# Optimization experiments

Hardware: AMD Instinct MI355X
Metric: run time of the kernel (lower is better)

Reference implementation:

```python
import jax, jax.numpy as jnp
import numpy as np

EPS = 1.0  # args.eps
N, D, H = 2097152, 2, 4

_PARAM_SPECS = [
    ("w_xin", (H, D)), ("b_xin", (H,)),
    ("w_xp1", (H, H)), ("b_xp1", (H,)),
    ("w_xp2", (H, H)), ("b_xp2", (H,)),
    ("w_xl1", (H, D)), ("b_xl1", (H,)),
    ("w_xl2", (H, H)), ("b_xl2", (H,)),
    ("w_xl3", (H, H)), ("b_xl3", (H,)),
    ("w_xlo", (1, H)), ("b_xlo", (1,)),
    ("w_cp1", (H, H)),  # PositiveLinear, no bias
    ("w_cp2", (H, H)),
    ("w_cpo", (1, H)),
    ("w_cp1m", (H, H)), ("b_cp1m", (H,)),
    ("w_cp2m", (H, H)), ("b_cp2m", (H,)),
    ("w_cpom", (H, H)), ("b_cpom", (H,)),
    ("w_clin", (H, D)),  # no bias
    ("w_cl1", (H, D)),
    ("w_cl2", (H, D)),
    ("w_clo", (1, D)),
    ("w_clinm", (D, D)), ("b_clinm", (D,)),
    ("w_cl1m", (D, H)), ("b_cl1m", (D,)),
    ("w_cl2m", (D, H)), ("b_cl2m", (D,)),
    ("w_clom", (D, H)), ("b_clom", (D,)),
]

def setup_inputs() -> dict:
    key = jax.random.key(0)
    k_x, k_xs, k_p = jax.random.split(key, 3)
    inp = {
        "x": jax.random.normal(k_x, (N, D), dtype=jnp.float32),
        "x_star": jax.random.normal(k_xs, (N, D), dtype=jnp.float32),
    }
    pkeys = jax.random.split(k_p, len(_PARAM_SPECS))
    for (name, shape), k in zip(_PARAM_SPECS, pkeys):
        if name.startswith("b_"):
            inp[name] = jnp.zeros(shape, dtype=jnp.float32)  # zeros bias init
        else:
            fan_in = shape[1]
            std = np.sqrt(2.0 / fan_in).astype(np.float32)  # kaiming normal
            inp[name] = jax.random.normal(k, shape, dtype=jnp.float32) * std
    return inp

def _lin(x, W, b=None):
    y = x @ W.T
    return y + b if b is not None else y

def _plin(x, W):
    # PositiveLinear reparam: W>=0 -> W + exp(-eps); W<0 -> exp(W - eps)
    Wr = jnp.where(W >= 0, W + jnp.exp(jnp.float32(-EPS)), jnp.exp(W - EPS))
    return x @ Wr.T

def reference(x, x_star,
              w_xin, b_xin, w_xp1, b_xp1, w_xp2, b_xp2,
              w_xl1, b_xl1, w_xl2, b_xl2, w_xl3, b_xl3, w_xlo, b_xlo,
              w_cp1, w_cp2, w_cpo,
              w_cp1m, b_cp1m, w_cp2m, b_cp2m, w_cpom, b_cpom,
              w_clin, w_cl1, w_cl2, w_clo,
              w_clinm, b_clinm, w_cl1m, b_cl1m, w_cl2m, b_cl2m, w_clom, b_clom):
    sp = jax.nn.softplus
    x0, x0s = x, x_star
    xs = sp(_lin(x0, w_xl1, b_xl1) + _lin(x0s * _lin(x0, w_clinm, b_clinm), w_clin))
    xh = sp(_lin(x0, w_xin, b_xin))
    xs = sp(_lin(xh, w_xl2, b_xl2)
            + _plin(xs * sp(_lin(xh, w_cp1m, b_cp1m)), w_cp1)
            + _lin(x0s * _lin(xh, w_cl1m, b_cl1m), w_cl1))
    xh = sp(_lin(xh, w_xp1, b_xp1))
    xs = sp(_lin(xh, w_xl3, b_xl3)
            + _plin(xs * sp(_lin(xh, w_cp2m, b_cp2m)), w_cp2)
            + _lin(x0s * _lin(xh, w_cl2m, b_cl2m), w_cl2))
    xh = sp(_lin(xh, w_xp2, b_xp2))
    out = sp(_lin(xh, w_xlo, b_xlo)
             + _plin(xs * sp(_lin(xh, w_cpom, b_cpom)), w_cpo)
             + _lin(x0s * _lin(xh, w_clom, b_clom), w_clo))
    return out  # [N, 1]
```

## Files before the change

kernel.cpp:

```cpp
#include <hip/hip_runtime.h>
#include <hip/hip_bf16.h>


#define NROWS_PER_THREAD 4

__device__ __forceinline__ float sp(float v) {
    float e = __expf(-fabsf(v));
    return fmaxf(v, 0.0f) + __logf(1.0f + e);
}

__device__ __forceinline__ float posw(float w) {
    const float EXP_NEG1 = 0.36787944117144233f;
    return (w >= 0.0f) ? (w + EXP_NEG1) : __expf(w - 1.0f);
}

__device__ __forceinline__ void mid_stage(
    float xs[NROWS_PER_THREAD][4], float xh[NROWS_PER_THREAD][4],
    const float XS0[NROWS_PER_THREAD][2],
    const float* __restrict__ w_xl,  const float* __restrict__ b_xl,
    const float* __restrict__ w_cpm, const float* __restrict__ b_cpm,
    const float* __restrict__ w_cp,
    const float* __restrict__ w_clm, const float* __restrict__ b_clm,
    const float* __restrict__ w_cl,
    const float* __restrict__ w_xp,  const float* __restrict__ b_xp)
{
    float v[NROWS_PER_THREAD][4];
    #pragma unroll
    for (int h = 0; h < 4; ++h) {
        float w0 = w_cpm[h*4+0], w1 = w_cpm[h*4+1], w2 = w_cpm[h*4+2], w3 = w_cpm[h*4+3];
        float b  = b_cpm[h];
        #pragma unroll
        for (int r = 0; r < NROWS_PER_THREAD; ++r) {
            float m = sp(fmaf(w0, xh[r][0], fmaf(w1, xh[r][1], fmaf(w2, xh[r][2], fmaf(w3, xh[r][3], b)))));
            v[r][h] = xs[r][h] * m;
        }
    }
    float u[NROWS_PER_THREAD][2];
    #pragma unroll
    for (int d = 0; d < 2; ++d) {
        float w0 = w_clm[d*4+0], w1 = w_clm[d*4+1], w2 = w_clm[d*4+2], w3 = w_clm[d*4+3];
        float b  = b_clm[d];
        #pragma unroll
        for (int r = 0; r < NROWS_PER_THREAD; ++r) {
            float t = fmaf(w0, xh[r][0], fmaf(w1, xh[r][1], fmaf(w2, xh[r][2], fmaf(w3, xh[r][3], b))));
            u[r][d] = XS0[r][d] * t;
        }
    }
    float ns[NROWS_PER_THREAD][4];
    #pragma unroll
    for (int h = 0; h < 4; ++h) {
        float a0 = w_xl[h*4+0], a1 = w_xl[h*4+1], a2 = w_xl[h*4+2], a3 = w_xl[h*4+3];
        float ab = b_xl[h];
        float p0 = posw(w_cp[h*4+0]), p1 = posw(w_cp[h*4+1]);
        float p2 = posw(w_cp[h*4+2]), p3 = posw(w_cp[h*4+3]);
        float c0 = w_cl[h*2+0], c1 = w_cl[h*2+1];
        #pragma unroll
        for (int r = 0; r < NROWS_PER_THREAD; ++r) {
            float t = fmaf(a0, xh[r][0], fmaf(a1, xh[r][1], fmaf(a2, xh[r][2], fmaf(a3, xh[r][3], ab))));
            t = fmaf(p0, v[r][0], fmaf(p1, v[r][1], fmaf(p2, v[r][2], fmaf(p3, v[r][3], t))));
            t = fmaf(c0, u[r][0], fmaf(c1, u[r][1], t));
            ns[r][h] = sp(t);
        }
    }
    float nh[NROWS_PER_THREAD][4];
    #pragma unroll
    for (int h = 0; h < 4; ++h) {
        float w0 = w_xp[h*4+0], w1 = w_xp[h*4+1], w2 = w_xp[h*4+2], w3 = w_xp[h*4+3];
        float b  = b_xp[h];
        #pragma unroll
        for (int r = 0; r < NROWS_PER_THREAD; ++r)
            nh[r][h] = sp(fmaf(w0, xh[r][0], fmaf(w1, xh[r][1], fmaf(w2, xh[r][2], fmaf(w3, xh[r][3], b)))));
    }
    #pragma unroll
    for (int r = 0; r < NROWS_PER_THREAD; ++r)
        #pragma unroll
        for (int h = 0; h < 4; ++h) { xs[r][h] = ns[r][h]; xh[r][h] = nh[r][h]; }
}

__global__ __launch_bounds__(256)
void dissip_kernel(
    const float* __restrict__ x,      const float* __restrict__ xst,
    const float* __restrict__ w_xin,  const float* __restrict__ b_xin,
    const float* __restrict__ w_xp1,  const float* __restrict__ b_xp1,
    const float* __restrict__ w_xp2,  const float* __restrict__ b_xp2,
    const float* __restrict__ w_xl1,  const float* __restrict__ b_xl1,
    const float* __restrict__ w_xl2,  const float* __restrict__ b_xl2,
    const float* __restrict__ w_xl3,  const float* __restrict__ b_xl3,
    const float* __restrict__ w_xlo,  const float* __restrict__ b_xlo,
    const float* __restrict__ w_cp1,  const float* __restrict__ w_cp2,
    const float* __restrict__ w_cpo,
    const float* __restrict__ w_cp1m, const float* __restrict__ b_cp1m,
    const float* __restrict__ w_cp2m, const float* __restrict__ b_cp2m,
    const float* __restrict__ w_cpom, const float* __restrict__ b_cpom,
    const float* __restrict__ w_clin, const float* __restrict__ w_cl1,
    const float* __restrict__ w_cl2,  const float* __restrict__ w_clo,
    const float* __restrict__ w_clinm,const float* __restrict__ b_clinm,
    const float* __restrict__ w_cl1m, const float* __restrict__ b_cl1m,
    const float* __restrict__ w_cl2m, const float* __restrict__ b_cl2m,
    const float* __restrict__ w_clom, const float* __restrict__ b_clom,
    float* __restrict__ out, int n)
{
    const int tid = blockIdx.x * blockDim.x + threadIdx.x;
    const int r0  = tid * NROWS_PER_THREAD;
    if (r0 >= n) return;
    const bool full = (r0 + NROWS_PER_THREAD <= n);

    float X0[NROWS_PER_THREAD][2], XS0[NROWS_PER_THREAD][2];
    if (full) {
        const float4 xa = *(const float4*)(x   + (size_t)r0 * 2);
        const float4 xb = *(const float4*)(x   + (size_t)r0 * 2 + 4);
        const float4 sa = *(const float4*)(xst + (size_t)r0 * 2);
        const float4 sb = *(const float4*)(xst + (size_t)r0 * 2 + 4);
        X0[0][0]=xa.x;  X0[0][1]=xa.y;  X0[1][0]=xa.z;  X0[1][1]=xa.w;
        X0[2][0]=xb.x;  X0[2][1]=xb.y;  X0[3][0]=xb.z;  X0[3][1]=xb.w;
        XS0[0][0]=sa.x; XS0[0][1]=sa.y; XS0[1][0]=sa.z; XS0[1][1]=sa.w;
        XS0[2][0]=sb.x; XS0[2][1]=sb.y; XS0[3][0]=sb.z; XS0[3][1]=sb.w;
    } else {
        #pragma unroll
        for (int r = 0; r < NROWS_PER_THREAD; ++r) {
            int row = r0 + r;
            if (row < n) {
                X0[r][0]  = x[(size_t)row*2];   X0[r][1]  = x[(size_t)row*2+1];
                XS0[r][0] = xst[(size_t)row*2]; XS0[r][1] = xst[(size_t)row*2+1];
            } else {
                X0[r][0] = X0[r][1] = XS0[r][0] = XS0[r][1] = 0.0f;
            }
        }
    }

    float xs[NROWS_PER_THREAD][4], xh[NROWS_PER_THREAD][4];

    float tcl[NROWS_PER_THREAD][2];
    #pragma unroll
    for (int d = 0; d < 2; ++d) {
        float w0 = w_clinm[d*2+0], w1 = w_clinm[d*2+1], b = b_clinm[d];
        #pragma unroll
        for (int r = 0; r < NROWS_PER_THREAD; ++r)
            tcl[r][d] = XS0[r][d] * fmaf(w0, X0[r][0], fmaf(w1, X0[r][1], b));
    }
    #pragma unroll
    for (int h = 0; h < 4; ++h) {
        float wl0 = w_xl1[h*2+0], wl1 = w_xl1[h*2+1], bl = b_xl1[h];
        float wc0 = w_clin[h*2+0], wc1 = w_clin[h*2+1];
        #pragma unroll
        for (int r = 0; r < NROWS_PER_THREAD; ++r) {
            float a = fmaf(wl0, X0[r][0], fmaf(wl1, X0[r][1], bl));
            a = fmaf(wc0, tcl[r][0], fmaf(wc1, tcl[r][1], a));
            xs[r][h] = sp(a);
        }
    }
    #pragma unroll
    for (int h = 0; h < 4; ++h) {
        float w0 = w_xin[h*2+0], w1 = w_xin[h*2+1], b = b_xin[h];
        #pragma unroll
        for (int r = 0; r < NROWS_PER_THREAD; ++r)
            xh[r][h] = sp(fmaf(w0, X0[r][0], fmaf(w1, X0[r][1], b)));
    }

    mid_stage(xs, xh, XS0, w_xl2, b_xl2, w_cp1m, b_cp1m, w_cp1, w_cl1m, b_cl1m, w_cl1, w_xp1, b_xp1);
    mid_stage(xs, xh, XS0, w_xl3, b_xl3, w_cp2m, b_cp2m, w_cp2, w_cl2m, b_cl2m, w_cl2, w_xp2, b_xp2);

    float o[NROWS_PER_THREAD];
    {
        float vv[NROWS_PER_THREAD][4];
        #pragma unroll
        for (int h = 0; h < 4; ++h) {
            float w0 = w_cpom[h*4+0], w1 = w_cpom[h*4+1], w2 = w_cpom[h*4+2], w3 = w_cpom[h*4+3];
            float b  = b_cpom[h];
            #pragma unroll
            for (int r = 0; r < NROWS_PER_THREAD; ++r) {
                float m = sp(fmaf(w0, xh[r][0], fmaf(w1, xh[r][1], fmaf(w2, xh[r][2], fmaf(w3, xh[r][3], b)))));
                vv[r][h] = xs[r][h] * m;
            }
        }
        float uu[NROWS_PER_THREAD][2];
        #pragma unroll
        for (int d = 0; d < 2; ++d) {
            float w0 = w_clom[d*4+0], w1 = w_clom[d*4+1], w2 = w_clom[d*4+2], w3 = w_clom[d*4+3];
            float b  = b_clom[d];
            #pragma unroll
            for (int r = 0; r < NROWS_PER_THREAD; ++r) {
                float t = fmaf(w0, xh[r][0], fmaf(w1, xh[r][1], fmaf(w2, xh[r][2], fmaf(w3, xh[r][3], b))));
                uu[r][d] = XS0[r][d] * t;
            }
        }
        float l0 = w_xlo[0], l1 = w_xlo[1], l2 = w_xlo[2], l3 = w_xlo[3], lb = b_xlo[0];
        float p0 = posw(w_cpo[0]), p1 = posw(w_cpo[1]), p2 = posw(w_cpo[2]), p3 = posw(w_cpo[3]);
        float c0 = w_clo[0], c1 = w_clo[1];
        #pragma unroll
        for (int r = 0; r < NROWS_PER_THREAD; ++r) {
            float t = fmaf(l0, xh[r][0], fmaf(l1, xh[r][1], fmaf(l2, xh[r][2], fmaf(l3, xh[r][3], lb))));
            t = fmaf(p0, vv[r][0], fmaf(p1, vv[r][1], fmaf(p2, vv[r][2], fmaf(p3, vv[r][3], t))));
            t = fmaf(c0, uu[r][0], fmaf(c1, uu[r][1], t));
            o[r] = sp(t);
        }
    }

    if (full) {
        *(float4*)(out + r0) = make_float4(o[0], o[1], o[2], o[3]);
    } else {
        #pragma unroll
        for (int r = 0; r < NROWS_PER_THREAD; ++r)
            if (r0 + r < n) out[r0 + r] = o[r];
    }
}

extern "C" void kernel_launch(void* const* d_in, const int* in_sizes, int n_in,
                              void* d_out, int out_size, void* d_ws, size_t ws_size,
                              hipStream_t stream) {
    const float* p[37];
    for (int i = 0; i < 37; ++i) p[i] = (const float*)d_in[i];
    const int n = in_sizes[0] / 2;
    const int threads = 256;
    const int rows_per_block = threads * NROWS_PER_THREAD;
    const int blocks = (n + rows_per_block - 1) / rows_per_block;

    dissip_kernel<<<dim3(blocks), dim3(threads), 0, stream>>>(
        p[0],  p[1],
        p[2],  p[3],  p[4],  p[5],  p[6],  p[7],
        p[8],  p[9],  p[10], p[11], p[12], p[13],
        p[14], p[15],
        p[16], p[17], p[18],
        p[19], p[20], p[21], p[22], p[23], p[24],
        p[25], p[26], p[27], p[28],
        p[29], p[30], p[31], p[32], p[33], p[34],
        p[35], p[36],
        (float*)d_out, n);
}
```

Before: 194.8 us.

## Prepack pre-scaled weights into workspace and evaluate softplus in base-2 domain

A one-block prep kernel copies every weight into a single contiguous workspace buffer, applies the PositiveLinear reparameterisation there, and pre-multiplies weights and biases by log2(e) or ln2. Softplus can then use the raw hardware exp2/log2 instructions without extra scaling multiplies, and the main kernel loads its weights from one pointer with constant offsets. Rows per thread drop from 4 to 2 and launch bounds request 4 blocks per CU to raise occupancy. The cost is an extra kernel launch per call and twice as many threads, each doing narrower vector loads and stores.

```diff
diff --git a/kernel.cpp b/kernel.cpp
--- a/kernel.cpp
+++ b/kernel.cpp
@@ -1,85 +1,23 @@
 #include <hip/hip_runtime.h>
-#include <hip/hip_bf16.h>
-
-
-#define NROWS_PER_THREAD 4
-
-__device__ __forceinline__ float sp(float v) {
-    float e = __expf(-fabsf(v));
-    return fmaxf(v, 0.0f) + __logf(1.0f + e);
+
+
+#define NR 2
+#define L2Ef 1.4426950408889634f
+#define LN2f 0.6931471805599453f
+
+__device__ __forceinline__ float sp2(float y) {
+    float e = __builtin_amdgcn_exp2f(-fabsf(y));
+    float l = __builtin_amdgcn_logf(1.0f + e);
+    return fmaxf(y, 0.0f) + l;
 }
 
 __device__ __forceinline__ float posw(float w) {
-    const float EXP_NEG1 = 0.36787944117144233f;
-    return (w >= 0.0f) ? (w + EXP_NEG1) : __expf(w - 1.0f);
-}
-
-__device__ __forceinline__ void mid_stage(
-    float xs[NROWS_PER_THREAD][4], float xh[NROWS_PER_THREAD][4],
-    const float XS0[NROWS_PER_THREAD][2],
-    const float* __restrict__ w_xl,  const float* __restrict__ b_xl,
-    const float* __restrict__ w_cpm, const float* __restrict__ b_cpm,
-    const float* __restrict__ w_cp,
-    const float* __restrict__ w_clm, const float* __restrict__ b_clm,
-    const float* __restrict__ w_cl,
-    const float* __restrict__ w_xp,  const float* __restrict__ b_xp)
-{
-    float v[NROWS_PER_THREAD][4];
-    #pragma unroll
-    for (int h = 0; h < 4; ++h) {
-        float w0 = w_cpm[h*4+0], w1 = w_cpm[h*4+1], w2 = w_cpm[h*4+2], w3 = w_cpm[h*4+3];
-        float b  = b_cpm[h];
-        #pragma unroll
-        for (int r = 0; r < NROWS_PER_THREAD; ++r) {
-            float m = sp(fmaf(w0, xh[r][0], fmaf(w1, xh[r][1], fmaf(w2, xh[r][2], fmaf(w3, xh[r][3], b)))));
-            v[r][h] = xs[r][h] * m;
-        }
-    }
-    float u[NROWS_PER_THREAD][2];
-    #pragma unroll
-    for (int d = 0; d < 2; ++d) {
-        float w0 = w_clm[d*4+0], w1 = w_clm[d*4+1], w2 = w_clm[d*4+2], w3 = w_clm[d*4+3];
-        float b  = b_clm[d];
-        #pragma unroll
-        for (int r = 0; r < NROWS_PER_THREAD; ++r) {
-            float t = fmaf(w0, xh[r][0], fmaf(w1, xh[r][1], fmaf(w2, xh[r][2], fmaf(w3, xh[r][3], b))));
-            u[r][d] = XS0[r][d] * t;
-        }
-    }
-    float ns[NROWS_PER_THREAD][4];
-    #pragma unroll
-    for (int h = 0; h < 4; ++h) {
-        float a0 = w_xl[h*4+0], a1 = w_xl[h*4+1], a2 = w_xl[h*4+2], a3 = w_xl[h*4+3];
-        float ab = b_xl[h];
-        float p0 = posw(w_cp[h*4+0]), p1 = posw(w_cp[h*4+1]);
-        float p2 = posw(w_cp[h*4+2]), p3 = posw(w_cp[h*4+3]);
-        float c0 = w_cl[h*2+0], c1 = w_cl[h*2+1];
-        #pragma unroll
-        for (int r = 0; r < NROWS_PER_THREAD; ++r) {
-            float t = fmaf(a0, xh[r][0], fmaf(a1, xh[r][1], fmaf(a2, xh[r][2], fmaf(a3, xh[r][3], ab))));
-            t = fmaf(p0, v[r][0], fmaf(p1, v[r][1], fmaf(p2, v[r][2], fmaf(p3, v[r][3], t))));
-            t = fmaf(c0, u[r][0], fmaf(c1, u[r][1], t));
-            ns[r][h] = sp(t);
-        }
-    }
-    float nh[NROWS_PER_THREAD][4];
-    #pragma unroll
-    for (int h = 0; h < 4; ++h) {
-        float w0 = w_xp[h*4+0], w1 = w_xp[h*4+1], w2 = w_xp[h*4+2], w3 = w_xp[h*4+3];
-        float b  = b_xp[h];
-        #pragma unroll
-        for (int r = 0; r < NROWS_PER_THREAD; ++r)
-            nh[r][h] = sp(fmaf(w0, xh[r][0], fmaf(w1, xh[r][1], fmaf(w2, xh[r][2], fmaf(w3, xh[r][3], b)))));
-    }
-    #pragma unroll
-    for (int r = 0; r < NROWS_PER_THREAD; ++r)
-        #pragma unroll
-        for (int h = 0; h < 4; ++h) { xs[r][h] = ns[r][h]; xh[r][h] = nh[r][h]; }
-}
+    return (w >= 0.0f) ? (w + 0.36787944117144233f) : __expf(w - 1.0f);
+}
+
 
 __global__ __launch_bounds__(256)
-void dissip_kernel(
-    const float* __restrict__ x,      const float* __restrict__ xst,
+void prep_kernel(
     const float* __restrict__ w_xin,  const float* __restrict__ b_xin,
     const float* __restrict__ w_xp1,  const float* __restrict__ b_xp1,
     const float* __restrict__ w_xp2,  const float* __restrict__ b_xp2,
@@ -98,109 +36,208 @@
     const float* __restrict__ w_cl1m, const float* __restrict__ b_cl1m,
     const float* __restrict__ w_cl2m, const float* __restrict__ b_cl2m,
     const float* __restrict__ w_clom, const float* __restrict__ b_clom,
-    float* __restrict__ out, int n)
+    float* __restrict__ wb)
+{
+    const int t = threadIdx.x;
+#define CPY(dst, src, cnt)    if (t < (cnt)) wb[(dst)+t] = src[t];
+#define SCL(dst, src, cnt, s) if (t < (cnt)) wb[(dst)+t] = (s) * src[t];
+#define PW(dst, src, cnt)     if (t < (cnt)) wb[(dst)+t] = LN2f * posw(src[t]);
+    SCL(0,   w_xl1,  8, L2Ef)
+    SCL(8,   b_xl1,  4, L2Ef)
+    SCL(12,  w_clin, 8, L2Ef)
+    CPY(20,  w_clinm,4)
+    CPY(24,  b_clinm,2)
+    SCL(26,  w_xin,  8, L2Ef)
+    SCL(34,  b_xin,  4, L2Ef)
+    CPY(38,  w_cp1m,16)
+    SCL(54,  b_cp1m, 4, L2Ef)
+    SCL(58,  w_cl1m, 8, LN2f)
+    CPY(66,  b_cl1m, 2)
+    CPY(68,  w_xl2, 16)
+    SCL(84,  b_xl2,  4, L2Ef)
+    PW (88,  w_cp1, 16)
+    SCL(104, w_cl1,  8, L2Ef)
+    CPY(112, w_xp1, 16)
+    SCL(128, b_xp1,  4, L2Ef)
+    CPY(132, w_cp2m,16)
+    SCL(148, b_cp2m, 4, L2Ef)
+    SCL(152, w_cl2m, 8, LN2f)
+    CPY(160, b_cl2m, 2)
+    CPY(162, w_xl3, 16)
+    SCL(178, b_xl3,  4, L2Ef)
+    PW (182, w_cp2, 16)
+    SCL(198, w_cl2,  8, L2Ef)
+    CPY(206, w_xp2, 16)
+    SCL(222, b_xp2,  4, L2Ef)
+    CPY(226, w_cpom,16)
+    SCL(242, b_cpom, 4, L2Ef)
+    SCL(246, w_clom, 8, LN2f)
+    CPY(254, b_clom, 2)
+    CPY(256, w_xlo,  4)
+    SCL(260, b_xlo,  1, L2Ef)
+    PW (261, w_cpo,  4)
+    SCL(265, w_clo,  2, L2Ef)
+#undef CPY
+#undef SCL
+#undef PW
+}
+
+__device__ __forceinline__ void mid_stage(
+    const float* __restrict__ wb,
+    float xs[NR][4], float xh[NR][4], const float XS0[NR][2])
+{
+    float v[NR][4];
+    #pragma unroll
+    for (int h = 0; h < 4; ++h) {
+        float w0 = wb[h*4+0], w1 = wb[h*4+1], w2 = wb[h*4+2], w3 = wb[h*4+3];
+        float b  = wb[16+h];
+        #pragma unroll
+        for (int r = 0; r < NR; ++r) {
+            float m = sp2(fmaf(w0, xh[r][0], fmaf(w1, xh[r][1], fmaf(w2, xh[r][2], fmaf(w3, xh[r][3], b)))));
+            v[r][h] = xs[r][h] * m;
+        }
+    }
+    float u[NR][2];
+    #pragma unroll
+    for (int d = 0; d < 2; ++d) {
+        float w0 = wb[20+d*4+0], w1 = wb[20+d*4+1], w2 = wb[20+d*4+2], w3 = wb[20+d*4+3];
+        float b  = wb[28+d];
+        #pragma unroll
+        for (int r = 0; r < NR; ++r) {
+            float t = fmaf(w0, xh[r][0], fmaf(w1, xh[r][1], fmaf(w2, xh[r][2], fmaf(w3, xh[r][3], b))));
+            u[r][d] = XS0[r][d] * t;
+        }
+    }
+    float ns[NR][4], nh[NR][4];
+    #pragma unroll
+    for (int h = 0; h < 4; ++h) {
+        float a0 = wb[30+h*4+0], a1 = wb[30+h*4+1], a2 = wb[30+h*4+2], a3 = wb[30+h*4+3];
+        float ab = wb[46+h];
+        float p0 = wb[50+h*4+0], p1 = wb[50+h*4+1], p2 = wb[50+h*4+2], p3 = wb[50+h*4+3];
+        float c0 = wb[66+h*2+0], c1 = wb[66+h*2+1];
+        #pragma unroll
+        for (int r = 0; r < NR; ++r) {
+            float t = fmaf(a0, xh[r][0], fmaf(a1, xh[r][1], fmaf(a2, xh[r][2], fmaf(a3, xh[r][3], ab))));
+            t = fmaf(p0, v[r][0], fmaf(p1, v[r][1], fmaf(p2, v[r][2], fmaf(p3, v[r][3], t))));
+            t = fmaf(c0, u[r][0], fmaf(c1, u[r][1], t));
+            ns[r][h] = sp2(t);
+        }
+    }
+    #pragma unroll
+    for (int h = 0; h < 4; ++h) {
+        float w0 = wb[74+h*4+0], w1 = wb[74+h*4+1], w2 = wb[74+h*4+2], w3 = wb[74+h*4+3];
+        float b  = wb[90+h];
+        #pragma unroll
+        for (int r = 0; r < NR; ++r)
+            nh[r][h] = sp2(fmaf(w0, xh[r][0], fmaf(w1, xh[r][1], fmaf(w2, xh[r][2], fmaf(w3, xh[r][3], b)))));
+    }
+    #pragma unroll
+    for (int r = 0; r < NR; ++r)
+        #pragma unroll
+        for (int h = 0; h < 4; ++h) { xs[r][h] = ns[r][h]; xh[r][h] = nh[r][h]; }
+}
+
+__global__ __launch_bounds__(256, 4)
+void dissip_main(const float* __restrict__ x, const float* __restrict__ xst,
+                 const float* __restrict__ wb, float* __restrict__ out, int n)
 {
     const int tid = blockIdx.x * blockDim.x + threadIdx.x;
-    const int r0  = tid * NROWS_PER_THREAD;
+    const int r0  = tid * NR;
     if (r0 >= n) return;
-    const bool full = (r0 + NROWS_PER_THREAD <= n);
-
-    float X0[NROWS_PER_THREAD][2], XS0[NROWS_PER_THREAD][2];
+    const bool full = (r0 + NR <= n);
+
+    float X0[NR][2], XS0[NR][2];
     if (full) {
         const float4 xa = *(const float4*)(x   + (size_t)r0 * 2);
-        const float4 xb = *(const float4*)(x   + (size_t)r0 * 2 + 4);
         const float4 sa = *(const float4*)(xst + (size_t)r0 * 2);
-        const float4 sb = *(const float4*)(xst + (size_t)r0 * 2 + 4);
         X0[0][0]=xa.x;  X0[0][1]=xa.y;  X0[1][0]=xa.z;  X0[1][1]=xa.w;
-        X0[2][0]=xb.x;  X0[2][1]=xb.y;  X0[3][0]=xb.z;  X0[3][1]=xb.w;
         XS0[0][0]=sa.x; XS0[0][1]=sa.y; XS0[1][0]=sa.z; XS0[1][1]=sa.w;
-        XS0[2][0]=sb.x; XS0[2][1]=sb.y; XS0[3][0]=sb.z; XS0[3][1]=sb.w;
     } else {
         #pragma unroll
-        for (int r = 0; r < NROWS_PER_THREAD; ++r) {
+        for (int r = 0; r < NR; ++r) {
             int row = r0 + r;
             if (row < n) {
                 X0[r][0]  = x[(size_t)row*2];   X0[r][1]  = x[(size_t)row*2+1];
                 XS0[r][0] = xst[(size_t)row*2]; XS0[r][1] = xst[(size_t)row*2+1];
-            } else {
-                X0[r][0] = X0[r][1] = XS0[r][0] = XS0[r][1] = 0.0f;
-            }
-        }
-    }
-
-    float xs[NROWS_PER_THREAD][4], xh[NROWS_PER_THREAD][4];
-
-    float tcl[NROWS_PER_THREAD][2];
-    #pragma unroll
-    for (int d = 0; d < 2; ++d) {
-        float w0 = w_clinm[d*2+0], w1 = w_clinm[d*2+1], b = b_clinm[d];
-        #pragma unroll
-        for (int r = 0; r < NROWS_PER_THREAD; ++r)
-            tcl[r][d] = XS0[r][d] * fmaf(w0, X0[r][0], fmaf(w1, X0[r][1], b));
-    }
-    #pragma unroll
-    for (int h = 0; h < 4; ++h) {
-        float wl0 = w_xl1[h*2+0], wl1 = w_xl1[h*2+1], bl = b_xl1[h];
-        float wc0 = w_clin[h*2+0], wc1 = w_clin[h*2+1];
-        #pragma unroll
-        for (int r = 0; r < NROWS_PER_THREAD; ++r) {
-            float a = fmaf(wl0, X0[r][0], fmaf(wl1, X0[r][1], bl));
-            a = fmaf(wc0, tcl[r][0], fmaf(wc1, tcl[r][1], a));
-            xs[r][h] = sp(a);
-        }
-    }
-    #pragma unroll
-    for (int h = 0; h < 4; ++h) {
-        float w0 = w_xin[h*2+0], w1 = w_xin[h*2+1], b = b_xin[h];
-        #pragma unroll
-        for (int r = 0; r < NROWS_PER_THREAD; ++r)
-            xh[r][h] = sp(fmaf(w0, X0[r][0], fmaf(w1, X0[r][1], b)));
-    }
-
-    mid_stage(xs, xh, XS0, w_xl2, b_xl2, w_cp1m, b_cp1m, w_cp1, w_cl1m, b_cl1m, w_cl1, w_xp1, b_xp1);
-    mid_stage(xs, xh, XS0, w_xl3, b_xl3, w_cp2m, b_cp2m, w_cp2, w_cl2m, b_cl2m, w_cl2, w_xp2, b_xp2);
-
-    float o[NROWS_PER_THREAD];
+            } else { X0[r][0]=X0[r][1]=XS0[r][0]=XS0[r][1]=0.0f; }
+        }
+    }
+
+    float xs[NR][4], xh[NR][4];
+
+    float tcl[NR][2];
     {
-        float vv[NROWS_PER_THREAD][4];
+        float m00=wb[20], m01=wb[21], m10=wb[22], m11=wb[23], c0=wb[24], c1=wb[25];
+        #pragma unroll
+        for (int r = 0; r < NR; ++r) {
+            tcl[r][0] = XS0[r][0] * fmaf(m00, X0[r][0], fmaf(m01, X0[r][1], c0));
+            tcl[r][1] = XS0[r][1] * fmaf(m10, X0[r][0], fmaf(m11, X0[r][1], c1));
+        }
+    }
+    #pragma unroll
+    for (int h = 0; h < 4; ++h) {
+        float a0 = wb[h*2+0], a1 = wb[h*2+1], ab = wb[8+h];
+        float c0 = wb[12+h*2+0], c1 = wb[12+h*2+1];
+        #pragma unroll
+        for (int r = 0; r < NR; ++r) {
+            float a = fmaf(a0, X0[r][0], fmaf(a1, X0[r][1], ab));
+            a = fmaf(c0, tcl[r][0], fmaf(c1, tcl[r][1], a));
+            xs[r][h] = sp2(a);
+        }
+    }
+    #pragma unroll
+    for (int h = 0; h < 4; ++h) {
+        float w0 = wb[26+h*2+0], w1 = wb[26+h*2+1], b = wb[34+h];
+        #pragma unroll
+        for (int r = 0; r < NR; ++r)
+            xh[r][h] = sp2(fmaf(w0, X0[r][0], fmaf(w1, X0[r][1], b)));
+    }
+
+    mid_stage(wb + 38,  xs, xh, XS0);
+    mid_stage(wb + 132, xs, xh, XS0);
+
+    float o[NR];
+    {
+        const float* ob = wb + 226;
+        float vv[NR][4];
         #pragma unroll
         for (int h = 0; h < 4; ++h) {
-            float w0 = w_cpom[h*4+0], w1 = w_cpom[h*4+1], w2 = w_cpom[h*4+2], w3 = w_cpom[h*4+3];
-            float b  = b_cpom[h];
+            float w0 = ob[h*4+0], w1 = ob[h*4+1], w2 = ob[h*4+2], w3 = ob[h*4+3];
+            float b  = ob[16+h];
             #pragma unroll
-            for (int r = 0; r < NROWS_PER_THREAD; ++r) {
-                float m = sp(fmaf(w0, xh[r][0], fmaf(w1, xh[r][1], fmaf(w2, xh[r][2], fmaf(w3, xh[r][3], b)))));
+            for (int r = 0; r < NR; ++r) {
+                float m = sp2(fmaf(w0, xh[r][0], fmaf(w1, xh[r][1], fmaf(w2, xh[r][2], fmaf(w3, xh[r][3], b)))));
                 vv[r][h] = xs[r][h] * m;
             }
         }
-        float uu[NROWS_PER_THREAD][2];
+        float uu[NR][2];
         #pragma unroll
         for (int d = 0; d < 2; ++d) {
-            float w0 = w_clom[d*4+0], w1 = w_clom[d*4+1], w2 = w_clom[d*4+2], w3 = w_clom[d*4+3];
-            float b  = b_clom[d];
+            float w0 = ob[20+d*4+0], w1 = ob[20+d*4+1], w2 = ob[20+d*4+2], w3 = ob[20+d*4+3];
+            float b  = ob[28+d];
             #pragma unroll
-            for (int r = 0; r < NROWS_PER_THREAD; ++r) {
+            for (int r = 0; r < NR; ++r) {
                 float t = fmaf(w0, xh[r][0], fmaf(w1, xh[r][1], fmaf(w2, xh[r][2], fmaf(w3, xh[r][3], b))));
                 uu[r][d] = XS0[r][d] * t;
             }
         }
-        float l0 = w_xlo[0], l1 = w_xlo[1], l2 = w_xlo[2], l3 = w_xlo[3], lb = b_xlo[0];
-        float p0 = posw(w_cpo[0]), p1 = posw(w_cpo[1]), p2 = posw(w_cpo[2]), p3 = posw(w_cpo[3]);
-        float c0 = w_clo[0], c1 = w_clo[1];
-        #pragma unroll
-        for (int r = 0; r < NROWS_PER_THREAD; ++r) {
+        float l0 = ob[30], l1 = ob[31], l2 = ob[32], l3 = ob[33], lb = ob[34];
+        float p0 = ob[35], p1 = ob[36], p2 = ob[37], p3 = ob[38];
+        float c0 = ob[39], c1 = ob[40];
+        #pragma unroll
+        for (int r = 0; r < NR; ++r) {
             float t = fmaf(l0, xh[r][0], fmaf(l1, xh[r][1], fmaf(l2, xh[r][2], fmaf(l3, xh[r][3], lb))));
             t = fmaf(p0, vv[r][0], fmaf(p1, vv[r][1], fmaf(p2, vv[r][2], fmaf(p3, vv[r][3], t))));
             t = fmaf(c0, uu[r][0], fmaf(c1, uu[r][1], t));
-            o[r] = sp(t);
+            o[r] = LN2f * sp2(t);
         }
     }
 
     if (full) {
-        *(float4*)(out + r0) = make_float4(o[0], o[1], o[2], o[3]);
+        *(float2*)(out + r0) = make_float2(o[0], o[1]);
     } else {
         #pragma unroll
-        for (int r = 0; r < NROWS_PER_THREAD; ++r)
+        for (int r = 0; r < NR; ++r)
             if (r0 + r < n) out[r0 + r] = o[r];
     }
 }
@@ -210,13 +247,10 @@
                               hipStream_t stream) {
     const float* p[37];
     for (int i = 0; i < 37; ++i) p[i] = (const float*)d_in[i];
+    float* wb = (float*)d_ws;
     const int n = in_sizes[0] / 2;
-    const int threads = 256;
-    const int rows_per_block = threads * NROWS_PER_THREAD;
-    const int blocks = (n + rows_per_block - 1) / rows_per_block;
-
-    dissip_kernel<<<dim3(blocks), dim3(threads), 0, stream>>>(
-        p[0],  p[1],
+
+    prep_kernel<<<dim3(1), dim3(256), 0, stream>>>(
         p[2],  p[3],  p[4],  p[5],  p[6],  p[7],
         p[8],  p[9],  p[10], p[11], p[12], p[13],
         p[14], p[15],
@@ -225,5 +259,11 @@
         p[25], p[26], p[27], p[28],
         p[29], p[30], p[31], p[32], p[33], p[34],
         p[35], p[36],
-        (float*)d_out, n);
-}
+        wb);
+
+    const int threads = 256;
+    const int rows_per_block = threads * NR;
+    const int blocks = (n + rows_per_block - 1) / rows_per_block;
+    dissip_main<<<dim3(blocks), dim3(threads), 0, stream>>>(
+        p[0], p[1], wb, (float*)d_out, n);
+}
```

Result: faster. 180.6 us (-7.3%).
